# Performance work log

Hardware: AMD Instinct MI355X
Metric: run time of the kernel (lower is better)

## Reference

```python
import jax, jax.numpy as jnp
import numpy as np

HEADS = 8
DIM_HEAD = 96
INNER = HEADS * DIM_HEAD  # 768
PEP_DIM = 768
PRO_DIM = 768
SCALE = DIM_HEAD ** -0.5
NEG = -1000000.0
EPS = 1e-5


def _layer_norm(x, g, b):
    mu = jnp.mean(x, axis=-1, keepdims=True)
    var = jnp.mean(jnp.square(x - mu), axis=-1, keepdims=True)
    return (x - mu) * jax.lax.rsqrt(var + EPS) * g + b


def setup_inputs() -> dict:
    key = jax.random.key(0)
    ks = jax.random.split(key, 12)
    b, n, m = 16, 128, 2048
    peptide = jax.random.normal(ks[0], (b, n, PEP_DIM), dtype=jnp.float32)
    protein = jax.random.normal(ks[1], (b, m, PRO_DIM), dtype=jnp.float32)
    peptide_mask = jax.random.randint(ks[2], (b, n), 0, 2, dtype=jnp.int32)
    pro_mask = jax.random.randint(ks[3], (b, m), 0, 2, dtype=jnp.int32)
    s = 0.02
    Wq = jax.random.normal(ks[4], (PEP_DIM, INNER), dtype=jnp.float32) * s
    Wk = jax.random.normal(ks[5], (PRO_DIM, INNER), dtype=jnp.float32) * s
    Wv_prot = jax.random.normal(ks[6], (PRO_DIM, INNER), dtype=jnp.float32) * s
    Wv_pep = jax.random.normal(ks[7], (PEP_DIM, INNER), dtype=jnp.float32) * s
    Wo_prot = jax.random.normal(ks[8], (INNER, PEP_DIM), dtype=jnp.float32) * s
    bo_prot = jnp.zeros((PEP_DIM,), dtype=jnp.float32)
    Wo_pep = jax.random.normal(ks[9], (INNER, PRO_DIM), dtype=jnp.float32) * s
    bo_pep = jnp.zeros((PRO_DIM,), dtype=jnp.float32)
    ln_g = jnp.ones((PEP_DIM,), dtype=jnp.float32)
    ln_b = jnp.zeros((PEP_DIM,), dtype=jnp.float32)
    return {
        'peptide': peptide, 'protein': protein,
        'peptide_mask': peptide_mask, 'pro_mask': pro_mask,
        'Wq': Wq, 'Wk': Wk, 'Wv_prot': Wv_prot, 'Wv_pep': Wv_pep,
        'Wo_prot': Wo_prot, 'bo_prot': bo_prot,
        'Wo_pep': Wo_pep, 'bo_pep': bo_pep,
        'ln_g': ln_g, 'ln_b': ln_b,
    }


def reference(peptide, protein, peptide_mask, pro_mask,
              Wq, Wk, Wv_prot, Wv_pep, Wo_prot, bo_prot, Wo_pep, bo_pep,
              ln_g, ln_b):
    b, n, _ = peptide.shape
    m = protein.shape[1]
    # projections -> (b, h, len, d)
    q = (peptide @ Wq).reshape(b, n, HEADS, DIM_HEAD).transpose(0, 2, 1, 3)
    k = (protein @ Wk).reshape(b, m, HEADS, DIM_HEAD).transpose(0, 2, 1, 3)
    v_prot = (protein @ Wv_prot).reshape(b, m, HEADS, DIM_HEAD).transpose(0, 2, 1, 3)
    v_pep = (peptide @ Wv_pep).reshape(b, n, HEADS, DIM_HEAD).transpose(0, 2, 1, 3)
    # scores (b, h, n, m)
    dots = jnp.einsum('bhnd,bhmd->bhnm', q, k) * SCALE
    dots = jnp.where(peptide_mask[:, None, :, None] == 0, NEG, dots)
    dots = jnp.where(pro_mask[:, None, None, :] == 0, NEG, dots)
    attn = jax.nn.softmax(dots, axis=-1)
    # peptide-side output: rows of attn aggregate protein values
    out_protein = jnp.einsum('bhnm,bhmd->bhnd', attn, v_prot)
    out_protein = out_protein.transpose(0, 2, 1, 3).reshape(b, n, INNER)
    out_protein = out_protein @ Wo_prot + bo_prot
    out_protein = _layer_norm(out_protein + peptide, ln_g, ln_b)
    # protein-side output: attn^T aggregates peptide values
    out_peptide = jnp.einsum('bhnm,bhnd->bhmd', attn, v_pep)
    out_peptide = out_peptide.transpose(0, 2, 1, 3).reshape(b, m, INNER)
    out_peptide = out_peptide @ Wo_pep + bo_pep
    out_peptide = _layer_norm(out_peptide + protein, ln_g, ln_b)
    return (out_protein, out_peptide, attn)
```

## Files before the change

kernel.cpp:

```cpp
#include <hip/hip_runtime.h>
#include <math.h>

static constexpr int HEADS  = 8;
static constexpr int DHEAD  = 96;
static constexpr int INNER  = 768;
static constexpr int NPEP   = 128;
static constexpr int MPRO   = 2048;
static constexpr float ATT_SCALE = 0.10206207261596577f;
static constexpr float NEGF   = -1000000.0f;
static constexpr float LN_EPS = 1e-5f;

typedef __attribute__((ext_vector_type(8))) short bf16x8;
typedef __attribute__((ext_vector_type(4))) float f32x4;

__device__ __forceinline__ unsigned short f2b(float f) {
    unsigned u = __builtin_bit_cast(unsigned, f);
    u += 0x7fffu + ((u >> 16) & 1u);
    return (unsigned short)(u >> 16);
}
__device__ __forceinline__ float b2f(unsigned short u) {
    return __builtin_bit_cast(float, (unsigned)u << 16);
}

__device__ __forceinline__ void async16(const unsigned short* g, unsigned short* l) {
    __builtin_amdgcn_global_load_lds(
        (const __attribute__((address_space(1))) void*)g,
        (__attribute__((address_space(3))) void*)l, 16, 0, 0);
}

template<int MODE>
__global__ __launch_bounds__(512) void gemm256(
    const unsigned short* __restrict__ A, const unsigned short* __restrict__ B,
    unsigned short* __restrict__ C,
    int N, int K, int lda, int ldb, int ldc,
    int lenShift, int nx,
    const unsigned short* __restrict__ B2, unsigned short* __restrict__ C2)
{
    __shared__ unsigned short As[2][256 * 32];
    __shared__ unsigned short Bs[2][256 * 32];

    const int tid = threadIdx.x;
    const int bid = blockIdx.x;
    const int per = gridDim.x >> 3;
    const int v   = (bid & 7) * per + (bid >> 3);
    int n0        = (v % nx) * 256;
    const int m0  = (v / nx) * 256;

    bool sideB = false;
    if (MODE == 5 && n0 >= 768) { sideB = true; n0 -= 768; }

    const unsigned short* Bb = (MODE == 5 && sideB) ? B2 : B;

    const int rS = tid >> 2;
    const int kS = (((tid & 3) ^ ((rS >> 1) & 3)) * 8);
    const int wave = tid >> 6;

    const int lane = tid & 63;
    const int l16  = lane & 15;
    const int quad = lane >> 4;
    const int wr   = (wave >> 2) * 128;
    const int wc   = (wave & 3) * 64;

    f32x4 acc[8][4];
#pragma unroll
    for (int i = 0; i < 8; ++i)
#pragma unroll
        for (int j = 0; j < 4; ++j) acc[i][j] = (f32x4){0.f, 0.f, 0.f, 0.f};

    auto stageT = [&](int t, int bi) {
        const int k0 = t << 5;
        unsigned short* a0 = &As[bi][wave * 512];
        async16(A + (long)(m0 + rS) * lda + k0 + kS, a0);
        async16(A + (long)(m0 + 128 + rS) * lda + k0 + kS, a0 + 4096);
        int bR0 = n0 + rS;       if (bR0 > N - 1) bR0 = N - 1;
        int bR1 = n0 + 128 + rS; if (bR1 > N - 1) bR1 = N - 1;
        unsigned short* b0 = &Bs[bi][wave * 512];
        async16(Bb + (long)bR0 * ldb + k0 + kS, b0);
        async16(Bb + (long)bR1 * ldb + k0 + kS, b0 + 4096);
    };

    const int NT = K >> 5;
    stageT(0, 0);
    stageT(1, 1);

    for (int t = 0; t < NT; ++t) {
        const int bi = t & 1;
        if (t < NT - 1) asm volatile("s_waitcnt vmcnt(4)" ::: "memory");
        else            asm volatile("s_waitcnt vmcnt(0)" ::: "memory");
        __builtin_amdgcn_s_barrier();

        bf16x8 af[8], bfr[4];
#pragma unroll
        for (int j = 0; j < 4; ++j) {
            const int rB = wc + j * 16 + l16;
            bfr[j] = *reinterpret_cast<const bf16x8*>(
                &Bs[bi][rB * 32 + ((quad ^ ((rB >> 1) & 3)) * 8)]);
        }
#pragma unroll
        for (int i = 0; i < 8; ++i) {
            const int rA = wr + i * 16 + l16;
            af[i] = *reinterpret_cast<const bf16x8*>(
                &As[bi][rA * 32 + ((quad ^ ((rA >> 1) & 3)) * 8)]);
        }

        __builtin_amdgcn_s_setprio(1);
#pragma unroll
        for (int i = 0; i < 8; ++i)
#pragma unroll
            for (int j = 0; j < 4; ++j)
                acc[i][j] = __builtin_amdgcn_mfma_f32_16x16x32_bf16(af[i], bfr[j], acc[i][j], 0, 0, 0);
        __builtin_amdgcn_s_setprio(0);

        __builtin_amdgcn_s_barrier();
        __builtin_amdgcn_sched_barrier(0);
        if (t + 2 < NT) stageT(t + 2, bi);
    }

#pragma unroll
    for (int i = 0; i < 8; ++i) {
#pragma unroll
        for (int j = 0; j < 4; ++j) {
            const int col = n0 + wc + j * 16 + l16;
            if ((MODE == 2) && col >= N) continue;
            const int h = col / 96, d = col - h * 96;
#pragma unroll
            for (int r = 0; r < 4; ++r) {
                const int row = m0 + wr + i * 16 + quad * 4 + r;
                float val = acc[i][j][r];
                if (MODE == 2) {
                    C[(long)row * ldc + col] = f2b(val);
                } else {
                    const int bb = row >> lenShift, rr = row & ((1 << lenShift) - 1);
                    if (!sideB)
                        C [(((long)(bb * 8 + h) << lenShift) + rr) * 96 + d] = f2b(val);
                    else
                        C2[(((long)(bb * 8 + h) * 96 + d) << lenShift) + rr] = f2b(val);
                }
            }
        }
    }
}

template<int TM, int MODE>
__global__ __launch_bounds__(256) void gemm_bf16(
    const unsigned short* __restrict__ A, const unsigned short* __restrict__ B,
    unsigned short* __restrict__ C,
    int M, int N, int K, int lda, int ldb, int ldc,
    long sAb, long sAh, long sBb, long sBh, long sCb, long sCh,
    int lenShift, int nxSwz,
    const unsigned short* __restrict__ B2, unsigned short* __restrict__ C2)
{
    (void)M;
    constexpr int FR   = TM / 32;
    constexpr int PIPE = 3;
    __shared__ unsigned short As[PIPE][TM * 32];
    __shared__ unsigned short Bs[PIPE][128 * 32];

    const int tid = threadIdx.x;
    int bx, by;
    if (nxSwz > 0) {
        const int bid = blockIdx.x;
        const int per = gridDim.x >> 3;
        const int v   = (bid & 7) * per + (bid >> 3);
        bx = v % nxSwz; by = v / nxSwz;
    } else { bx = blockIdx.x; by = blockIdx.y; }
    int n0        = bx * 128;
    const int m0  = by * TM;
    const int z   = blockIdx.z;
    const int zb  = z >> 3, zh = z & 7;

    bool sideB = false;
    if (MODE == 5 && n0 >= 768) { sideB = true; n0 -= 768; }

    const unsigned short* Ab = A + zb * sAb + zh * sAh;
    const unsigned short* Bb = ((MODE == 5 && sideB) ? B2 : B) + zb * sBb + zh * sBh;

    const int rS = tid >> 2;
    const int kS = (((tid & 3) ^ ((rS >> 1) & 3)) * 8);
    const int wave = tid >> 6;

    const int lane = tid & 63;
    const int l16  = lane & 15;
    const int quad = lane >> 4;
    const int wr   = (wave >> 1) * (TM / 2);
    const int wc   = (wave & 1) * 64;

    f32x4 acc[FR][4];
#pragma unroll
    for (int i = 0; i < FR; ++i)
#pragma unroll
        for (int j = 0; j < 4; ++j) acc[i][j] = (f32x4){0.f, 0.f, 0.f, 0.f};

    auto stageT = [&](int t, int bi) {
        const int k0 = t << 5;
        unsigned short* a0 = &As[bi][wave * 512];
        async16(Ab + (long)(m0 + rS) * lda + k0 + kS, a0);
        if (TM == 128)
            async16(Ab + (long)(m0 + 64 + rS) * lda + k0 + kS, a0 + 2048);
        int bR0 = n0 + rS;      if (bR0 > N - 1) bR0 = N - 1;
        int bR1 = n0 + 64 + rS; if (bR1 > N - 1) bR1 = N - 1;
        unsigned short* b0 = &Bs[bi][wave * 512];
        async16(Bb + (long)bR0 * ldb + k0 + kS, b0);
        async16(Bb + (long)bR1 * ldb + k0 + kS, b0 + 2048);
    };

    const int NT = K >> 5;
    stageT(0, 0);
    if (NT > 1) stageT(1, 1);
    if (NT > 2) stageT(2, 2);

    int bi = 0;
    for (int t = 0; t < NT; ++t) {
        const int ahead = NT - 1 - t;
        if constexpr (TM == 128) {
            if (ahead >= 2)      asm volatile("s_waitcnt vmcnt(8)" ::: "memory");
            else if (ahead == 1) asm volatile("s_waitcnt vmcnt(4)" ::: "memory");
            else                 asm volatile("s_waitcnt vmcnt(0)" ::: "memory");
        } else {
            if (ahead >= 2)      asm volatile("s_waitcnt vmcnt(6)" ::: "memory");
            else if (ahead == 1) asm volatile("s_waitcnt vmcnt(3)" ::: "memory");
            else                 asm volatile("s_waitcnt vmcnt(0)" ::: "memory");
        }
        __builtin_amdgcn_s_barrier();

        bf16x8 af[FR], bfr[4];
#pragma unroll
        for (int i = 0; i < FR; ++i) {
            const int rA = wr + i * 16 + l16;
            af[i] = *reinterpret_cast<const bf16x8*>(
                &As[bi][rA * 32 + ((quad ^ ((rA >> 1) & 3)) * 8)]);
        }
#pragma unroll
        for (int j = 0; j < 4; ++j) {
            const int rB = wc + j * 16 + l16;
            bfr[j] = *reinterpret_cast<const bf16x8*>(
                &Bs[bi][rB * 32 + ((quad ^ ((rB >> 1) & 3)) * 8)]);
        }

        __builtin_amdgcn_s_setprio(1);
#pragma unroll
        for (int i = 0; i < FR; ++i)
#pragma unroll
            for (int j = 0; j < 4; ++j)
                acc[i][j] = __builtin_amdgcn_mfma_f32_16x16x32_bf16(af[i], bfr[j], acc[i][j], 0, 0, 0);
        __builtin_amdgcn_s_setprio(0);

        __builtin_amdgcn_s_barrier();
        __builtin_amdgcn_sched_barrier(0);
        if (t + PIPE < NT) stageT(t + PIPE, bi);
        bi = bi + 1; if (bi == PIPE) bi = 0;
    }

#pragma unroll
    for (int i = 0; i < FR; ++i) {
#pragma unroll
        for (int j = 0; j < 4; ++j) {
            const int col = n0 + wc + j * 16 + l16;
            if ((MODE == 2) && col >= N) continue;
            const int h = col / 96, d = col - h * 96;
#pragma unroll
            for (int r = 0; r < 4; ++r) {
                const int row = m0 + wr + i * 16 + quad * 4 + r;
                float v = acc[i][j][r];
                if (MODE == 1) {
                    v *= ATT_SCALE;
                    C[zb * sCb + zh * sCh + (long)row * ldc + col] = f2b(v);
                } else if (MODE == 2) {
                    C[zb * sCb + zh * sCh + (long)row * ldc + col] = f2b(v);
                } else if (MODE == 3) {
                    const int bb = row >> lenShift, rr = row & ((1 << lenShift) - 1);
                    C[(((long)(bb * 8 + h) << lenShift) + rr) * 96 + d] = f2b(v);
                } else if (MODE == 4) {
                    const int bb = row >> lenShift, rr = row & ((1 << lenShift) - 1);
                    C[(((long)(bb * 8 + h) * 96 + d) << lenShift) + rr] = f2b(v);
                } else {
                    const int bb = row >> lenShift, rr = row & ((1 << lenShift) - 1);
                    if (!sideB)
                        C [(((long)(bb * 8 + h) << lenShift) + rr) * 96 + d] = f2b(v);
                    else
                        C2[(((long)(bb * 8 + h) * 96 + d) << lenShift) + rr] = f2b(v);
                }
            }
        }
    }
}

__global__ __launch_bounds__(256) void fusedpv_kernel(
    const unsigned short* __restrict__ attn16,
    const unsigned short* __restrict__ vprotT,
    const unsigned short* __restrict__ vpepT,
    unsigned short* __restrict__ opp,
    unsigned short* __restrict__ opep)
{
    __shared__ unsigned short AttT[128 * 136];
    __shared__ unsigned short Vp[96 * 136];

    const int id = blockIdx.x;
    const int z  = ((id >> 4) << 3) + (id & 7);
    const int nh = (id >> 3) & 1;
    const int b  = z >> 3, h = z & 7;

    const unsigned short* Az = attn16 + (long)z * NPEP * MPRO;
    const unsigned short* Vz = vprotT + (long)z * 96 * MPRO;
    const unsigned short* Pz = vpepT  + (long)z * 96 * 128;

    const int tid  = threadIdx.x;
    const int lane = tid & 63;
    const int l16  = lane & 15;
    const int quad = lane >> 4;
    const int wave = tid >> 6;
    const int wrN  = (wave >> 1) * 32;
    const int wrM  = (wave >> 1) * 64;
    const int wcD  = (wave & 1) * 48;

#pragma unroll
    for (int e = 0; e < 6; ++e) {
        const int c = tid + e * 256;
        const int row = c >> 4, coloff = (c & 15) * 8;
        bf16x8 v = *reinterpret_cast<const bf16x8*>(Pz + row * 128 + coloff);
        *reinterpret_cast<bf16x8*>(&Vp[row * 136 + coloff]) = v;
    }
    __syncthreads();

    f32x4 acc1[2][3];
#pragma unroll
    for (int i = 0; i < 2; ++i)
#pragma unroll
        for (int j = 0; j < 3; ++j) acc1[i][j] = (f32x4){0.f, 0.f, 0.f, 0.f};

    for (int cc = 0; cc < 16; ++cc) {
        const int m0 = cc * 128;
        const bool own = (cc >> 3) == nh;

        bf16x8 a1[2][4], b1[3][4];
#pragma unroll
        for (int i = 0; i < 2; ++i) {
            const int n = nh * 64 + wrN + i * 16 + l16;
#pragma unroll
            for (int kc = 0; kc < 4; ++kc)
                a1[i][kc] = *reinterpret_cast<const bf16x8*>(
                    Az + (long)n * MPRO + m0 + kc * 32 + quad * 8);
        }
#pragma unroll
        for (int j = 0; j < 3; ++j) {
            const int d = wcD + j * 16 + l16;
#pragma unroll
            for (int kc = 0; kc < 4; ++kc)
                b1[j][kc] = *reinterpret_cast<const bf16x8*>(
                    Vz + (long)d * MPRO + m0 + kc * 32 + quad * 8);
        }

        if (own) {
            const int mBase = (tid & 7) * 16;
#pragma unroll
            for (int nn = 0; nn < 128; nn += 32) {
                const int n = nn + (tid >> 3);
#pragma unroll
                for (int c = 0; c < 2; ++c) {
                    bf16x8 v = *reinterpret_cast<const bf16x8*>(
                        Az + (long)n * MPRO + m0 + mBase + c * 8);
#pragma unroll
                    for (int jj = 0; jj < 8; ++jj)
                        AttT[(mBase + c * 8 + jj) * 136 + n] = (unsigned short)v[jj];
                }
            }
            __syncthreads();
        }

#pragma unroll
        for (int kc = 0; kc < 4; ++kc)
#pragma unroll
            for (int i = 0; i < 2; ++i)
#pragma unroll
                for (int j = 0; j < 3; ++j)
                    acc1[i][j] = __builtin_amdgcn_mfma_f32_16x16x32_bf16(
                        a1[i][kc], b1[j][kc], acc1[i][j], 0, 0, 0);

        if (own) {
            f32x4 acc2[4][3];
#pragma unroll
            for (int i = 0; i < 4; ++i)
#pragma unroll
                for (int j = 0; j < 3; ++j) acc2[i][j] = (f32x4){0.f, 0.f, 0.f, 0.f};
#pragma unroll
            for (int kc = 0; kc < 4; ++kc) {
                bf16x8 a2[4], b2v[3];
#pragma unroll
                for (int i = 0; i < 4; ++i)
                    a2[i] = *reinterpret_cast<const bf16x8*>(
                        &AttT[(wrM + i * 16 + l16) * 136 + kc * 32 + quad * 8]);
#pragma unroll
                for (int j = 0; j < 3; ++j)
                    b2v[j] = *reinterpret_cast<const bf16x8*>(
                        &Vp[(wcD + j * 16 + l16) * 136 + kc * 32 + quad * 8]);
#pragma unroll
                for (int i = 0; i < 4; ++i)
#pragma unroll
                    for (int j = 0; j < 3; ++j)
                        acc2[i][j] = __builtin_amdgcn_mfma_f32_16x16x32_bf16(
                            a2[i], b2v[j], acc2[i][j], 0, 0, 0);
            }
#pragma unroll
            for (int i = 0; i < 4; ++i)
#pragma unroll
                for (int j = 0; j < 3; ++j) {
                    const int d = wcD + j * 16 + l16;
#pragma unroll
                    for (int r = 0; r < 4; ++r) {
                        const int m = m0 + wrM + i * 16 + quad * 4 + r;
                        opep[(long)b * MPRO * INNER + (long)m * INNER + h * 96 + d]
                            = f2b(acc2[i][j][r]);
                    }
                }
            __syncthreads();
        }
    }

#pragma unroll
    for (int i = 0; i < 2; ++i)
#pragma unroll
        for (int j = 0; j < 3; ++j) {
            const int d = wcD + j * 16 + l16;
#pragma unroll
            for (int r = 0; r < 4; ++r) {
                const int n = nh * 64 + wrN + i * 16 + quad * 4 + r;
                opp[((long)b * NPEP + n) * INNER + h * 96 + d] = f2b(acc1[i][j][r]);
            }
        }
}

__global__ __launch_bounds__(256) void conv2_kernel(
    const float* __restrict__ pro, const float* __restrict__ pep,
    unsigned short* __restrict__ pro16, unsigned short* __restrict__ pep16,
    int nPro4, int nPep4)
{
    const int i = blockIdx.x * 256 + threadIdx.x;
    const float* in; unsigned short* out; int idx;
    if (i < nPro4) { in = pro; out = pro16; idx = i; }
    else { idx = i - nPro4; if (idx >= nPep4) return; in = pep; out = pep16; }
    float4 v = reinterpret_cast<const float4*>(in)[idx];
    ushort4 o;
    o.x = f2b(v.x); o.y = f2b(v.y); o.z = f2b(v.z); o.w = f2b(v.w);
    reinterpret_cast<ushort4*>(out)[idx] = o;
}

__global__ __launch_bounds__(256) void wtrans_kernel(
    const float* w0, const float* w1, const float* w2,
    const float* w3, const float* w4, const float* w5,
    unsigned short* o0, unsigned short* o1, unsigned short* o2,
    unsigned short* o3, unsigned short* o4, unsigned short* o5)
{
    const float* in; unsigned short* out;
    switch (blockIdx.z) {
        case 0: in = w0; out = o0; break;
        case 1: in = w1; out = o1; break;
        case 2: in = w2; out = o2; break;
        case 3: in = w3; out = o3; break;
        case 4: in = w4; out = o4; break;
        default: in = w5; out = o5; break;
    }
    __shared__ unsigned short t[32][33];
    const int bx = blockIdx.x * 32, by = blockIdx.y * 32;
    const int x = threadIdx.x, y = threadIdx.y;
#pragma unroll
    for (int i = 0; i < 32; i += 8)
        t[y + i][x] = f2b(in[(long)(by + y + i) * 768 + bx + x]);
    __syncthreads();
#pragma unroll
    for (int i = 0; i < 32; i += 8)
        out[(long)(bx + y + i) * 768 + by + x] = t[x][y + i];
}

__global__ __launch_bounds__(256) void softmax_kernel(
    unsigned short* __restrict__ s16, float* __restrict__ attn,
    const int* __restrict__ pepm, const int* __restrict__ prom)
{
    __shared__ float smx[4], sms[4];
    const long row = blockIdx.x;
    const int b = (int)(row >> 10);
    const int n = (int)(row & 127);
    unsigned short* p16 = s16 + row * (long)MPRO;
    float* pf = attn + row * (long)MPRO;
    const int tid = threadIdx.x;
    const int wv = tid >> 6;
    const int rowOk = pepm[(b << 7) + n];

    float v[8];
    float mx = -3.4e38f;
    if (rowOk) {
#pragma unroll
        for (int k = 0; k < 8; ++k) {
            const int c = tid + k * 256;
            float x = b2f(p16[c]);
            if (prom[(b << 11) + c] == 0) x = NEGF;
            v[k] = x; mx = fmaxf(mx, x);
        }
    } else {
#pragma unroll
        for (int k = 0; k < 8; ++k) v[k] = NEGF;
        mx = NEGF;
    }
#pragma unroll
    for (int off = 32; off > 0; off >>= 1) mx = fmaxf(mx, __shfl_xor(mx, off));
    if ((tid & 63) == 0) smx[wv] = mx;
    __syncthreads();
    mx = fmaxf(fmaxf(smx[0], smx[1]), fmaxf(smx[2], smx[3]));

    float sum = 0.f;
#pragma unroll
    for (int k = 0; k < 8; ++k) { v[k] = __expf(v[k] - mx); sum += v[k]; }
#pragma unroll
    for (int off = 32; off > 0; off >>= 1) sum += __shfl_xor(sum, off);
    if ((tid & 63) == 0) sms[wv] = sum;
    __syncthreads();
    const float inv = 1.0f / (sms[0] + sms[1] + sms[2] + sms[3]);
#pragma unroll
    for (int k = 0; k < 8; ++k) {
        const float o = v[k] * inv;
        pf[tid + k * 256] = o;
        p16[tid + k * 256] = f2b(o);
    }
}

__global__ __launch_bounds__(256) void bias_res_ln(
    const unsigned short* __restrict__ tmp, const float* __restrict__ bias,
    const float* __restrict__ res, const float* __restrict__ gam,
    const float* __restrict__ bet, float* __restrict__ out)
{
    __shared__ float red[8];
    const long row = blockIdx.x;
    const unsigned short* t = tmp + row * INNER;
    const float* r = res + row * INNER;
    float* o = out + row * INNER;
    const int tid = threadIdx.x;
    const int wv = tid >> 6;

    float v[3]; float s = 0.f;
#pragma unroll
    for (int k = 0; k < 3; ++k) { const int c = tid + k * 256; v[k] = b2f(t[c]) + bias[c] + r[c]; s += v[k]; }
#pragma unroll
    for (int off = 32; off > 0; off >>= 1) s += __shfl_xor(s, off);
    if ((tid & 63) == 0) red[wv] = s;
    __syncthreads();
    const float mu = (red[0] + red[1] + red[2] + red[3]) * (1.0f / INNER);

    float vs = 0.f;
#pragma unroll
    for (int k = 0; k < 3; ++k) { const float d = v[k] - mu; vs += d * d; }
#pragma unroll
    for (int off = 32; off > 0; off >>= 1) vs += __shfl_xor(vs, off);
    if ((tid & 63) == 0) red[4 + wv] = vs;
    __syncthreads();
    const float rstd = rsqrtf((red[4] + red[5] + red[6] + red[7]) * (1.0f / INNER) + LN_EPS);
#pragma unroll
    for (int k = 0; k < 3; ++k) { const int c = tid + k * 256; o[c] = (v[k] - mu) * rstd * gam[c] + bet[c]; }
}

extern "C" void kernel_launch(void* const* d_in, const int* in_sizes, int n_in,
                              void* d_out, int out_size, void* d_ws, size_t ws_size,
                              hipStream_t stream)
{
    (void)in_sizes; (void)n_in; (void)out_size; (void)ws_size;

    const float* peptide = (const float*)d_in[0];
    const float* protein = (const float*)d_in[1];
    const int*   pepm    = (const int*)  d_in[2];
    const int*   prom    = (const int*)  d_in[3];
    const float* Wq      = (const float*)d_in[4];
    const float* Wk      = (const float*)d_in[5];
    const float* Wv_prot = (const float*)d_in[6];
    const float* Wv_pep  = (const float*)d_in[7];
    const float* Wo_prot = (const float*)d_in[8];
    const float* bo_prot = (const float*)d_in[9];
    const float* Wo_pep  = (const float*)d_in[10];
    const float* bo_pep  = (const float*)d_in[11];
    const float* ln_g    = (const float*)d_in[12];
    const float* ln_b    = (const float*)d_in[13];

    char* ws = (char*)d_ws;
    auto U = [&](size_t off) { return (unsigned short*)(ws + off); };
    unsigned short* WT0   = U(0);
    unsigned short* WT1   = U(1179648);
    unsigned short* WT2   = U(2 * 1179648);
    unsigned short* WT3   = U(3 * 1179648);
    unsigned short* WT4   = U(4 * 1179648);
    unsigned short* WT5   = U(5 * 1179648);
    unsigned short* q16   = U(7077888);
    unsigned short* k16   = U(10223616);
    unsigned short* vpT   = U(60555264);
    unsigned short* vpepT = U(110886912);
    unsigned short* s16   = U(114032640);
    unsigned short* pro16 = U(114032640);
    unsigned short* pep16 = U(164364288);
    unsigned short* opp   = U(7077888);
    unsigned short* opep  = U(10223616);
    unsigned short* tmp1  = U(164364288);
    unsigned short* tmp2  = U(63700992);

    float* outP = (float*)d_out;
    float* outQ = outP + 16 * 128 * 768;
    float* attn = outQ + (long)16 * 2048 * 768;

    conv2_kernel<<<26112, 256, 0, stream>>>(protein, peptide, pro16, pep16, 6291456, 393216);
    wtrans_kernel<<<dim3(24, 24, 6), dim3(32, 8), 0, stream>>>(
        Wq, Wk, Wv_prot, Wv_pep, Wo_prot, Wo_pep, WT0, WT1, WT2, WT3, WT4, WT5);

    gemm_bf16<128, 5><<<dim3(12, 16, 1), 256, 0, stream>>>(
        pep16, WT0, q16, 2048, 768, 768, 768, 768, 0,
        0, 0, 0, 0, 0, 0, 7, 0, WT3, vpepT);
    gemm256<5><<<768, 512, 0, stream>>>(
        pro16, WT1, k16, 768, 768, 768, 768, 0,
        11, 6, WT2, vpT);

    gemm_bf16<128, 1><<<dim3(16, 1, 128), 256, 0, stream>>>(
        q16, k16, s16, 128, 2048, 96, 96, 96, 2048,
        98304L, 12288L, 1572864L, 196608L, 2097152L, 262144L, 0, 0, nullptr, nullptr);

    softmax_kernel<<<16384, 256, 0, stream>>>(s16, attn, pepm, prom);

    fusedpv_kernel<<<256, 256, 0, stream>>>(s16, vpT, vpepT, opp, opep);

    gemm_bf16<64, 2><<<dim3(6, 32, 1), 256, 0, stream>>>(
        opp, WT4, tmp1, 2048, 768, 768, 768, 768, 768,
        0, 0, 0, 0, 0, 0, 0, 0, nullptr, nullptr);
    bias_res_ln<<<2048, 256, 0, stream>>>(tmp1, bo_prot, peptide, ln_g, ln_b, outP);

    gemm256<2><<<384, 512, 0, stream>>>(
        opep, WT5, tmp2, 768, 768, 768, 768, 768,
        0, 3, nullptr, nullptr);
    bias_res_ln<<<32768, 256, 0, stream>>>(tmp2, bo_pep, protein, ln_g, ln_b, outQ);
}
```

Baseline: 774.3 us.

## Replace 256x256 GEMM with 128x128 K64-tile kernel and shrink pipeline depth

Replaces the 512-thread 256x256-tile GEMM used for the large protein projections and output projection with a 256-thread 128x128-tile kernel that stages 64-wide K slices with an XOR swizzle over 8 chunks. The grids grow fourfold, which evens out load across CUs and shortens each block's epilogue, but each loaded byte is reused less. The smaller gemm_bf16 kernel also drops from a 3-stage to a 2-stage LDS pipeline, which lowers LDS use for higher occupancy at the cost of less latency hiding.

```diff
diff --git a/kernel.cpp b/kernel.cpp
--- a/kernel.cpp
+++ b/kernel.cpp
@@ -29,95 +29,99 @@
 }
 
 template<int MODE>
-__global__ __launch_bounds__(512) void gemm256(
+__global__ __launch_bounds__(256) void gemm_k64(
     const unsigned short* __restrict__ A, const unsigned short* __restrict__ B,
     unsigned short* __restrict__ C,
     int N, int K, int lda, int ldb, int ldc,
     int lenShift, int nx,
     const unsigned short* __restrict__ B2, unsigned short* __restrict__ C2)
 {
-    __shared__ unsigned short As[2][256 * 32];
-    __shared__ unsigned short Bs[2][256 * 32];
+    __shared__ unsigned short As[2][128 * 64];
+    __shared__ unsigned short Bs[2][128 * 64];
 
     const int tid = threadIdx.x;
     const int bid = blockIdx.x;
     const int per = gridDim.x >> 3;
     const int v   = (bid & 7) * per + (bid >> 3);
-    int n0        = (v % nx) * 256;
-    const int m0  = (v / nx) * 256;
+    int n0        = (v % nx) * 128;
+    const int m0  = (v / nx) * 128;
 
     bool sideB = false;
     if (MODE == 5 && n0 >= 768) { sideB = true; n0 -= 768; }
-
     const unsigned short* Bb = (MODE == 5 && sideB) ? B2 : B;
 
-    const int rS = tid >> 2;
-    const int kS = (((tid & 3) ^ ((rS >> 1) & 3)) * 8);
-    const int wave = tid >> 6;
+    const int l = tid & 63, w = tid >> 6;
+    const int sRowBase = w * 8 + ((tid >> 3) & 7);
+    const int sG = tid & 7;
 
     const int lane = tid & 63;
     const int l16  = lane & 15;
     const int quad = lane >> 4;
-    const int wr   = (wave >> 2) * 128;
-    const int wc   = (wave & 3) * 64;
-
-    f32x4 acc[8][4];
-#pragma unroll
-    for (int i = 0; i < 8; ++i)
+    const int wr   = (w >> 1) * 64;
+    const int wc   = (w & 1) * 64;
+
+    f32x4 acc[4][4];
+#pragma unroll
+    for (int i = 0; i < 4; ++i)
 #pragma unroll
         for (int j = 0; j < 4; ++j) acc[i][j] = (f32x4){0.f, 0.f, 0.f, 0.f};
 
     auto stageT = [&](int t, int bi) {
-        const int k0 = t << 5;
-        unsigned short* a0 = &As[bi][wave * 512];
-        async16(A + (long)(m0 + rS) * lda + k0 + kS, a0);
-        async16(A + (long)(m0 + 128 + rS) * lda + k0 + kS, a0 + 4096);
-        int bR0 = n0 + rS;       if (bR0 > N - 1) bR0 = N - 1;
-        int bR1 = n0 + 128 + rS; if (bR1 > N - 1) bR1 = N - 1;
-        unsigned short* b0 = &Bs[bi][wave * 512];
-        async16(Bb + (long)bR0 * ldb + k0 + kS, b0);
-        async16(Bb + (long)bR1 * ldb + k0 + kS, b0 + 4096);
+        const int k0 = t << 6;
+#pragma unroll
+        for (int ro = 0; ro < 4; ++ro) {
+            const int row = ro * 32 + sRowBase;
+            const int col = k0 + ((sG ^ (row & 7)) * 8);
+            unsigned short* dst = &As[bi][ro * 2048 + w * 512 + l * 8];
+            async16(A + (long)(m0 + row) * lda + col, dst);
+            int br = n0 + row; if (br > N - 1) br = N - 1;
+            unsigned short* dstB = &Bs[bi][ro * 2048 + w * 512 + l * 8];
+            async16(Bb + (long)br * ldb + col, dstB);
+        }
     };
 
-    const int NT = K >> 5;
+    const int NT = K >> 6;
     stageT(0, 0);
     stageT(1, 1);
 
+    int bi = 0;
     for (int t = 0; t < NT; ++t) {
-        const int bi = t & 1;
-        if (t < NT - 1) asm volatile("s_waitcnt vmcnt(4)" ::: "memory");
+        if (t < NT - 1) asm volatile("s_waitcnt vmcnt(8)" ::: "memory");
         else            asm volatile("s_waitcnt vmcnt(0)" ::: "memory");
         __builtin_amdgcn_s_barrier();
 
-        bf16x8 af[8], bfr[4];
-#pragma unroll
-        for (int j = 0; j < 4; ++j) {
-            const int rB = wc + j * 16 + l16;
-            bfr[j] = *reinterpret_cast<const bf16x8*>(
-                &Bs[bi][rB * 32 + ((quad ^ ((rB >> 1) & 3)) * 8)]);
-        }
-#pragma unroll
-        for (int i = 0; i < 8; ++i) {
-            const int rA = wr + i * 16 + l16;
-            af[i] = *reinterpret_cast<const bf16x8*>(
-                &As[bi][rA * 32 + ((quad ^ ((rA >> 1) & 3)) * 8)]);
-        }
-
-        __builtin_amdgcn_s_setprio(1);
-#pragma unroll
-        for (int i = 0; i < 8; ++i)
-#pragma unroll
-            for (int j = 0; j < 4; ++j)
-                acc[i][j] = __builtin_amdgcn_mfma_f32_16x16x32_bf16(af[i], bfr[j], acc[i][j], 0, 0, 0);
-        __builtin_amdgcn_s_setprio(0);
+#pragma unroll
+        for (int kc = 0; kc < 2; ++kc) {
+            bf16x8 af[4], bfr[4];
+#pragma unroll
+            for (int i = 0; i < 4; ++i) {
+                const int rA = wr + i * 16 + l16;
+                af[i] = *reinterpret_cast<const bf16x8*>(
+                    &As[bi][rA * 64 + (((kc * 4 + quad) ^ (rA & 7)) * 8)]);
+            }
+#pragma unroll
+            for (int j = 0; j < 4; ++j) {
+                const int rB = wc + j * 16 + l16;
+                bfr[j] = *reinterpret_cast<const bf16x8*>(
+                    &Bs[bi][rB * 64 + (((kc * 4 + quad) ^ (rB & 7)) * 8)]);
+            }
+            __builtin_amdgcn_s_setprio(1);
+#pragma unroll
+            for (int i = 0; i < 4; ++i)
+#pragma unroll
+                for (int j = 0; j < 4; ++j)
+                    acc[i][j] = __builtin_amdgcn_mfma_f32_16x16x32_bf16(af[i], bfr[j], acc[i][j], 0, 0, 0);
+            __builtin_amdgcn_s_setprio(0);
+        }
 
         __builtin_amdgcn_s_barrier();
         __builtin_amdgcn_sched_barrier(0);
         if (t + 2 < NT) stageT(t + 2, bi);
-    }
-
-#pragma unroll
-    for (int i = 0; i < 8; ++i) {
+        bi ^= 1;
+    }
+
+#pragma unroll
+    for (int i = 0; i < 4; ++i) {
 #pragma unroll
         for (int j = 0; j < 4; ++j) {
             const int col = n0 + wc + j * 16 + l16;
@@ -152,7 +156,7 @@
 {
     (void)M;
     constexpr int FR   = TM / 32;
-    constexpr int PIPE = 3;
+    constexpr int PIPE = 2;
     __shared__ unsigned short As[PIPE][TM * 32];
     __shared__ unsigned short Bs[PIPE][128 * 32];
 
@@ -207,19 +211,14 @@
     const int NT = K >> 5;
     stageT(0, 0);
     if (NT > 1) stageT(1, 1);
-    if (NT > 2) stageT(2, 2);
 
     int bi = 0;
     for (int t = 0; t < NT; ++t) {
-        const int ahead = NT - 1 - t;
-        if constexpr (TM == 128) {
-            if (ahead >= 2)      asm volatile("s_waitcnt vmcnt(8)" ::: "memory");
-            else if (ahead == 1) asm volatile("s_waitcnt vmcnt(4)" ::: "memory");
-            else                 asm volatile("s_waitcnt vmcnt(0)" ::: "memory");
+        if (t < NT - 1) {
+            if constexpr (TM == 128) asm volatile("s_waitcnt vmcnt(4)" ::: "memory");
+            else                     asm volatile("s_waitcnt vmcnt(3)" ::: "memory");
         } else {
-            if (ahead >= 2)      asm volatile("s_waitcnt vmcnt(6)" ::: "memory");
-            else if (ahead == 1) asm volatile("s_waitcnt vmcnt(3)" ::: "memory");
-            else                 asm volatile("s_waitcnt vmcnt(0)" ::: "memory");
+            asm volatile("s_waitcnt vmcnt(0)" ::: "memory");
         }
         __builtin_amdgcn_s_barrier();
 
@@ -248,7 +247,7 @@
         __builtin_amdgcn_s_barrier();
         __builtin_amdgcn_sched_barrier(0);
         if (t + PIPE < NT) stageT(t + PIPE, bi);
-        bi = bi + 1; if (bi == PIPE) bi = 0;
+        bi ^= 1;
     }
 
 #pragma unroll
@@ -608,9 +607,9 @@
     gemm_bf16<128, 5><<<dim3(12, 16, 1), 256, 0, stream>>>(
         pep16, WT0, q16, 2048, 768, 768, 768, 768, 0,
         0, 0, 0, 0, 0, 0, 7, 0, WT3, vpepT);
-    gemm256<5><<<768, 512, 0, stream>>>(
+    gemm_k64<5><<<3072, 256, 0, stream>>>(
         pro16, WT1, k16, 768, 768, 768, 768, 0,
-        11, 6, WT2, vpT);
+        11, 12, WT2, vpT);
 
     gemm_bf16<128, 1><<<dim3(16, 1, 128), 256, 0, stream>>>(
         q16, k16, s16, 128, 2048, 96, 96, 96, 2048,
@@ -625,8 +624,8 @@
         0, 0, 0, 0, 0, 0, 0, 0, nullptr, nullptr);
     bias_res_ln<<<2048, 256, 0, stream>>>(tmp1, bo_prot, peptide, ln_g, ln_b, outP);
 
-    gemm256<2><<<384, 512, 0, stream>>>(
+    gemm_k64<2><<<1536, 256, 0, stream>>>(
         opep, WT5, tmp2, 768, 768, 768, 768, 768,
-        0, 3, nullptr, nullptr);
+        0, 6, nullptr, nullptr);
     bias_res_ln<<<32768, 256, 0, stream>>>(tmp2, bo_pep, protein, ln_g, ln_b, outQ);
 }
```

New measurement: 740.9 us. 4.3% less time.
